# Kernel tuning notes

Hardware: AMD Instinct MI355X
Metric: run time of the kernel (lower is better)

## Reference

```python
import jax, jax.numpy as jnp
import numpy as np

B, C, G = 2, 256, 32
SPATIAL = (16, 16, 16)
EPS = 1e-5


def setup_inputs() -> dict:
    key = jax.random.key(0)
    ks = jax.random.split(key, 11)
    s = 1.0 / np.sqrt(C)
    x = jax.random.normal(ks[0], (B, C) + SPATIAL, dtype=jnp.float32)
    mk = lambda k: jax.random.normal(k, (C, C), dtype=jnp.float32) * s
    return {
        "x": x,
        "Wq": mk(ks[1]), "bq": jnp.zeros((C,), jnp.float32),
        "Wk": mk(ks[2]), "bk": jnp.zeros((C,), jnp.float32),
        "Wv": mk(ks[3]), "bv": jnp.zeros((C,), jnp.float32),
        "Wo": mk(ks[4]), "bo": jnp.zeros((C,), jnp.float32),
        "gamma": jnp.ones((C,), jnp.float32),
        "beta": jnp.zeros((C,), jnp.float32),
    }


def reference(x, Wq, bq, Wk, bk, Wv, bv, Wo, bo, gamma, beta):
    b, c = x.shape[0], x.shape[1]
    xf = x.reshape(b, c, -1)  # [B, C, N]

    def proj1x1(inp, W, bias):
        return jnp.einsum('oc,bcn->bon', W, inp) + bias[None, :, None]

    q = proj1x1(xf, Wq, bq)
    k = proj1x1(xf, Wk, bk)
    v = proj1x1(xf, Wv, bv)

    # qk[b, n, m] = sum_c q[b, c, n] * k[b, c, m]   (no 1/sqrt(C) scale, as in source)
    scores = jnp.einsum('bcn,bcm->bnm', q, k)
    w = jax.nn.softmax(scores, axis=-1)
    # h[b, c, n] = sum_m v[b, c, m] * w[b, n, m]
    h = jnp.einsum('bcm,bnm->bcn', v, w)
    h = proj1x1(h, Wo, bo)

    y = xf + h  # residual

    # GroupNorm over (channels-in-group, spatial)
    yg = y.reshape(b, G, c // G, -1)
    mu = jnp.mean(yg, axis=(2, 3), keepdims=True)
    var = jnp.var(yg, axis=(2, 3), keepdims=True)
    yn = ((yg - mu) * jax.lax.rsqrt(var + EPS)).reshape(b, c, -1)
    yn = yn * gamma[None, :, None] + beta[None, :, None]

    out = yn * jax.nn.sigmoid(yn)  # SiLU
    return out.reshape(x.shape)
```

## Files before the change

kernel.cpp:

```cpp
#include <hip/hip_runtime.h>
#include <hip/hip_bf16.h>

typedef _Float16 f16;
typedef __attribute__((ext_vector_type(4))) _Float16 f16x4;
typedef __attribute__((ext_vector_type(8))) _Float16 f16x8;
typedef __attribute__((ext_vector_type(4))) float f32x4;

#define CD 256
#define ND 4096
#define GD 32
#define KVB 32

__device__ __forceinline__ void gl_lds16(const f16* g, f16* l) {
    __builtin_amdgcn_global_load_lds(
        (const __attribute__((address_space(1))) unsigned int*)g,
        (__attribute__((address_space(3))) unsigned int*)l,
        16, 0, 0);
}

__global__ __launch_bounds__(256)
void k_proj_qkv(const float* __restrict__ x,
                const float* __restrict__ Wq, const float* __restrict__ bq,
                const float* __restrict__ Wk, const float* __restrict__ bk,
                const float* __restrict__ Wv, const float* __restrict__ bv,
                f16* __restrict__ Qt, f16* __restrict__ Kt, f16* __restrict__ Vb)
{
    __shared__ f16 As[3][64][40];
    __shared__ f16 Bs[64][40];
    __shared__ f16 Ts[64][72];

    const int t  = threadIdx.x;
    const int n0 = blockIdx.x * 64;
    const int o0 = blockIdx.y * 64;
    const int bb = blockIdx.z;

    const float* Ws[3] = { Wq, Wk, Wv };
    const float* bs[3] = { bq, bk, bv };

    const int w  = t >> 6;
    const int l  = t & 63;
    const int lr = l & 15;
    const int lg = l >> 4;
    const int wo = (w >> 1) * 32;
    const int wn = (w & 1) * 32;

    const int sl = t & 63;
    const int k8 = (t >> 6) * 8;

    f32x4 acc[3][2][2] = {};

    for (int ck = 0; ck < CD; ck += 32) {
        __syncthreads();
#pragma unroll
        for (int p = 0; p < 3; ++p) {
            const float* s = Ws[p] + (size_t)(o0 + sl) * CD + ck + k8;
            f16x8 v;
#pragma unroll
            for (int u = 0; u < 8; ++u) v[u] = (f16)s[u];
            *(f16x8*)&As[p][sl][k8] = v;
        }
        {
            const float* s = x + ((size_t)bb * CD + ck + k8) * ND + n0 + sl;
            f16x8 v;
#pragma unroll
            for (int u = 0; u < 8; ++u) v[u] = (f16)s[(size_t)u * ND];
            *(f16x8*)&Bs[sl][k8] = v;
        }
        __syncthreads();
        f16x8 b0 = *(const f16x8*)&Bs[wn + lr][lg * 8];
        f16x8 b1 = *(const f16x8*)&Bs[wn + 16 + lr][lg * 8];
#pragma unroll
        for (int p = 0; p < 3; ++p) {
            f16x8 a0 = *(const f16x8*)&As[p][wo + lr][lg * 8];
            f16x8 a1 = *(const f16x8*)&As[p][wo + 16 + lr][lg * 8];
            acc[p][0][0] = __builtin_amdgcn_mfma_f32_16x16x32_f16(a0, b0, acc[p][0][0], 0, 0, 0);
            acc[p][0][1] = __builtin_amdgcn_mfma_f32_16x16x32_f16(a0, b1, acc[p][0][1], 0, 0, 0);
            acc[p][1][0] = __builtin_amdgcn_mfma_f32_16x16x32_f16(a1, b0, acc[p][1][0], 0, 0, 0);
            acc[p][1][1] = __builtin_amdgcn_mfma_f32_16x16x32_f16(a1, b1, acc[p][1][1], 0, 0, 0);
        }
    }

#pragma unroll
    for (int p = 0; p < 2; ++p) {
        __syncthreads();
#pragma unroll
        for (int so = 0; so < 2; ++so)
#pragma unroll
            for (int r = 0; r < 4; ++r) {
                int orow  = wo + so * 16 + lg * 4 + r;
                float bv_ = bs[p][o0 + orow];
#pragma unroll
                for (int sn = 0; sn < 2; ++sn)
                    Ts[orow][wn + sn * 16 + lr] = (f16)(acc[p][so][sn][r] + bv_);
            }
        __syncthreads();
        f16* dst = (p == 0) ? Qt : Kt;
        int n  = t >> 2;
        int o8 = (t & 3) * 16;
        f16 tmp[16];
#pragma unroll
        for (int u = 0; u < 16; ++u) tmp[u] = Ts[o8 + u][n];
        f16* g = dst + ((size_t)bb * ND + n0 + n) * CD + o0 + o8;
        *(f16x8*)g       = *(f16x8*)&tmp[0];
        *(f16x8*)(g + 8) = *(f16x8*)&tmp[8];
    }
#pragma unroll
    for (int so = 0; so < 2; ++so)
#pragma unroll
        for (int r = 0; r < 4; ++r) {
            int orow  = wo + so * 16 + lg * 4 + r;
            float bv_ = bv[o0 + orow];
#pragma unroll
            for (int sn = 0; sn < 2; ++sn) {
                int ncol = wn + sn * 16 + lr;
                Vb[((size_t)bb * CD + o0 + orow) * ND + n0 + ncol] =
                    (f16)(acc[2][so][sn][r] + bv_);
            }
        }
}

template<int KSN>
__global__ __launch_bounds__(256, 2)
void k_attn(const f16* __restrict__ Qt, const f16* __restrict__ Kt,
            const f16* __restrict__ Vb, f16* __restrict__ Op,
            float* __restrict__ ml)
{
    __shared__ f16 Ks[2][32 * 256];
    __shared__ f16 Vs[2][256 * 32];
    __shared__ f16 Pl[4][32][40];

    const int t  = threadIdx.x;
    const int w  = t >> 6;
    const int l  = t & 63;
    const int lr = l & 15;
    const int lg = l >> 4;

    const int bid = blockIdx.x;
    int bb, ks, qi;
    if constexpr (KSN == 8) {
        int xcd = bid & 7;
        bb = xcd & 1;
        ks = (xcd >> 1) | ((bid >> 8) << 2);
        qi = (bid >> 3) & 31;
    } else {
        bb = bid & 1;
        ks = (bid >> 1) & 3;
        qi = bid >> 3;
    }
    const int q0 = qi * 128 + w * 32;

    f16x8 qf[2][8];
#pragma unroll
    for (int qs = 0; qs < 2; ++qs)
#pragma unroll
        for (int kc = 0; kc < 8; ++kc)
            qf[qs][kc] = *(const f16x8*)(Qt + ((size_t)bb * ND + q0 + qs * 16 + lr) * CD + kc * 32 + lg * 8);

    f32x4 oacc[2][16] = {};
    float row_m[2] = { -3.0e38f, -3.0e38f };
    float row_l[2] = { 0.f, 0.f };

    const int kv0 = ks * (ND / KSN);
    const f16* ktb = Kt + (size_t)bb * ND * CD;
    const f16* vbb = Vb + (size_t)bb * CD * ND;

    int koff[4], voff[4];
#pragma unroll
    for (int j = 0; j < 4; ++j) {
        int v   = (w * 4 + j) * 64 + l;
        int row = v >> 5;
        int ch  = (v & 31) ^ (row & 7);
        koff[j] = row * CD + ch * 8;
        int c   = v >> 2;
        int u   = (v & 3) ^ ((c >> 1) & 3);
        voff[j] = c * ND + u * 8;
    }

    auto stage = [&](int m0, int bi) {
#pragma unroll
        for (int j = 0; j < 4; ++j)
            gl_lds16(ktb + (size_t)m0 * CD + koff[j], &Ks[bi][(w * 4 + j) * 512]);
#pragma unroll
        for (int j = 0; j < 4; ++j)
            gl_lds16(vbb + m0 + voff[j], &Vs[bi][(w * 4 + j) * 512]);
    };

    stage(kv0, 0);
    __syncthreads();

    const int NIT = (ND / KSN) / KVB;
    for (int it = 0; it < NIT; ++it) {
        const int bi = it & 1;
        if (it + 1 < NIT) stage(kv0 + (it + 1) * KVB, bi ^ 1);

        f32x4 s[2][2] = {};
        __builtin_amdgcn_s_setprio(1);
#pragma unroll
        for (int kc = 0; kc < 8; ++kc) {
            int chs = ((kc * 4 + lg) ^ (lr & 7)) * 8;
            f16x8 k0 = *(const f16x8*)&Ks[bi][(lr) * 256 + chs];
            f16x8 k1 = *(const f16x8*)&Ks[bi][(16 + lr) * 256 + chs];
            s[0][0] = __builtin_amdgcn_mfma_f32_16x16x32_f16(k0, qf[0][kc], s[0][0], 0, 0, 0);
            s[1][0] = __builtin_amdgcn_mfma_f32_16x16x32_f16(k1, qf[0][kc], s[1][0], 0, 0, 0);
            s[0][1] = __builtin_amdgcn_mfma_f32_16x16x32_f16(k0, qf[1][kc], s[0][1], 0, 0, 0);
            s[1][1] = __builtin_amdgcn_mfma_f32_16x16x32_f16(k1, qf[1][kc], s[1][1], 0, 0, 0);
        }
        __builtin_amdgcn_s_setprio(0);

#pragma unroll
        for (int qs = 0; qs < 2; ++qs) {
            float pm = fmaxf(
                fmaxf(fmaxf(s[0][qs][0], s[0][qs][1]), fmaxf(s[0][qs][2], s[0][qs][3])),
                fmaxf(fmaxf(s[1][qs][0], s[1][qs][1]), fmaxf(s[1][qs][2], s[1][qs][3])));
            pm = fmaxf(pm, __shfl_xor(pm, 16));
            pm = fmaxf(pm, __shfl_xor(pm, 32));
            bool need = (pm > row_m[qs] + 5.0f);
            float nm  = need ? pm : row_m[qs];
            float p0 = __expf(s[0][qs][0] - nm);
            float p1 = __expf(s[0][qs][1] - nm);
            float p2 = __expf(s[0][qs][2] - nm);
            float p3 = __expf(s[0][qs][3] - nm);
            float p4 = __expf(s[1][qs][0] - nm);
            float p5 = __expf(s[1][qs][1] - nm);
            float p6 = __expf(s[1][qs][2] - nm);
            float p7 = __expf(s[1][qs][3] - nm);
            float ps = ((p0 + p1) + (p2 + p3)) + ((p4 + p5) + (p6 + p7));
            ps += __shfl_xor(ps, 16);
            ps += __shfl_xor(ps, 32);
            if (__any(need)) {
                float sc = __expf(row_m[qs] - nm);
                row_l[qs] = row_l[qs] * sc + ps;
#pragma unroll
                for (int ct = 0; ct < 16; ++ct) {
                    oacc[qs][ct][0] *= sc; oacc[qs][ct][1] *= sc;
                    oacc[qs][ct][2] *= sc; oacc[qs][ct][3] *= sc;
                }
            } else {
                row_l[qs] += ps;
            }
            row_m[qs] = nm;
            f16x4 pk0 = { (f16)p0, (f16)p1, (f16)p2, (f16)p3 };
            f16x4 pk1 = { (f16)p4, (f16)p5, (f16)p6, (f16)p7 };
            *(f16x4*)&Pl[w][qs * 16 + lr][lg * 4]      = pk0;
            *(f16x4*)&Pl[w][qs * 16 + lr][16 + lg * 4] = pk1;
        }

        f16x8 pf0 = *(const f16x8*)&Pl[w][lr][lg * 8];
        f16x8 pf1 = *(const f16x8*)&Pl[w][16 + lr][lg * 8];
        __builtin_amdgcn_s_setprio(1);
#pragma unroll
        for (int ct = 0; ct < 16; ++ct) {
            f16x8 vf = *(const f16x8*)&Vs[bi][(ct * 16 + lr) * 32 + ((lg ^ ((lr >> 1) & 3))) * 8];
            oacc[0][ct] = __builtin_amdgcn_mfma_f32_16x16x32_f16(vf, pf0, oacc[0][ct], 0, 0, 0);
            oacc[1][ct] = __builtin_amdgcn_mfma_f32_16x16x32_f16(vf, pf1, oacc[1][ct], 0, 0, 0);
        }
        __builtin_amdgcn_s_setprio(0);
        __syncthreads();
    }

#pragma unroll
    for (int qs = 0; qs < 2; ++qs)
#pragma unroll
        for (int ct = 0; ct < 16; ++ct)
#pragma unroll
            for (int r = 0; r < 4; ++r) {
                int cch = ct * 16 + lg * 4 + r;
                Op[(((size_t)ks * 2 + bb) * CD + cch) * ND + q0 + qs * 16 + lr] =
                    (f16)oacc[qs][ct][r];
            }
    if (lg == 0) {
#pragma unroll
        for (int qs = 0; qs < 2; ++qs) {
            int n = q0 + qs * 16 + lr;
            ml[((ks * 2 + bb) * 2 + 0) * ND + n] = row_m[qs];
            ml[((ks * 2 + bb) * 2 + 1) * ND + n] = row_l[qs];
        }
    }
}

template<int KSN>
__global__ __launch_bounds__(256)
void k_ml(const float* __restrict__ ml, float* __restrict__ wq)
{
    int i = blockIdx.x * 256 + threadIdx.x;
    int b = i / ND, n = i % ND;
    float m[KSN], lv[KSN];
#pragma unroll
    for (int ks = 0; ks < KSN; ++ks) {
        m[ks]  = ml[((ks * 2 + b) * 2 + 0) * ND + n];
        lv[ks] = ml[((ks * 2 + b) * 2 + 1) * ND + n];
    }
    float M = m[0];
#pragma unroll
    for (int ks = 1; ks < KSN; ++ks) M = fmaxf(M, m[ks]);
    float wgt[KSN], L = 0.f;
#pragma unroll
    for (int ks = 0; ks < KSN; ++ks) { wgt[ks] = __expf(m[ks] - M); L += wgt[ks] * lv[ks]; }
    float inv = 1.0f / L;
#pragma unroll
    for (int ks = 0; ks < KSN; ++ks)
        wq[(ks * 2 + b) * ND + n] = wgt[ks] * inv;
}

template<int KSN>
__global__ __launch_bounds__(256)
void k_comb(const f16* __restrict__ Op, const float* __restrict__ wq,
            f16* __restrict__ Hb)
{
    size_t i = (size_t)blockIdx.x * 256 + threadIdx.x;
    int n0 = (int)(i % (ND / 8)) * 8;
    int c  = (int)((i / (ND / 8)) % CD);
    int b  = (int)(i / ((size_t)CD * (ND / 8)));

    float acc[8] = {};
#pragma unroll
    for (int ks = 0; ks < KSN; ++ks) {
        f16x8 o = *(const f16x8*)(Op + (((size_t)ks * 2 + b) * CD + c) * ND + n0);
        const float* wp = wq + (ks * 2 + b) * ND + n0;
        float4 w0 = *(const float4*)wp;
        float4 w1 = *(const float4*)(wp + 4);
        acc[0] += w0.x * (float)o[0]; acc[1] += w0.y * (float)o[1];
        acc[2] += w0.z * (float)o[2]; acc[3] += w0.w * (float)o[3];
        acc[4] += w1.x * (float)o[4]; acc[5] += w1.y * (float)o[5];
        acc[6] += w1.z * (float)o[6]; acc[7] += w1.w * (float)o[7];
    }
    f16x8 h;
#pragma unroll
    for (int u = 0; u < 8; ++u) h[u] = (f16)acc[u];
    *(f16x8*)(Hb + ((size_t)b * CD + c) * ND + n0) = h;
}

__global__ __launch_bounds__(256)
void k_proj_o(const f16* __restrict__ Hb, const float* __restrict__ Wo,
              const float* __restrict__ bo, const float* __restrict__ x,
              f16* __restrict__ Yh, float* __restrict__ part)
{
    __shared__ f16 As[64][40];
    __shared__ f16 Bs[64][40];
    __shared__ float rs[4][2][2][2];

    const int t  = threadIdx.x;
    const int n0 = blockIdx.x * 64;
    const int o0 = blockIdx.y * 64;
    const int bb = blockIdx.z;

    const int w  = t >> 6;
    const int l  = t & 63;
    const int lr = l & 15;
    const int lg = l >> 4;
    const int wo = (w >> 1) * 32;
    const int wn = (w & 1) * 32;

    const int sl = t & 63;
    const int k8 = (t >> 6) * 8;

    f32x4 acc[2][2] = {};

    for (int ck = 0; ck < CD; ck += 32) {
        __syncthreads();
        {
            const float* s = Wo + (size_t)(o0 + sl) * CD + ck + k8;
            f16x8 v;
#pragma unroll
            for (int u = 0; u < 8; ++u) v[u] = (f16)s[u];
            *(f16x8*)&As[sl][k8] = v;
        }
        {
            const f16* s = Hb + ((size_t)bb * CD + ck + k8) * ND + n0 + sl;
            f16x8 v;
#pragma unroll
            for (int u = 0; u < 8; ++u) v[u] = s[(size_t)u * ND];
            *(f16x8*)&Bs[sl][k8] = v;
        }
        __syncthreads();
        f16x8 a0 = *(const f16x8*)&As[wo + lr][lg * 8];
        f16x8 a1 = *(const f16x8*)&As[wo + 16 + lr][lg * 8];
        f16x8 b0 = *(const f16x8*)&Bs[wn + lr][lg * 8];
        f16x8 b1 = *(const f16x8*)&Bs[wn + 16 + lr][lg * 8];
        acc[0][0] = __builtin_amdgcn_mfma_f32_16x16x32_f16(a0, b0, acc[0][0], 0, 0, 0);
        acc[0][1] = __builtin_amdgcn_mfma_f32_16x16x32_f16(a0, b1, acc[0][1], 0, 0, 0);
        acc[1][0] = __builtin_amdgcn_mfma_f32_16x16x32_f16(a1, b0, acc[1][0], 0, 0, 0);
        acc[1][1] = __builtin_amdgcn_mfma_f32_16x16x32_f16(a1, b1, acc[1][1], 0, 0, 0);
    }

#pragma unroll
    for (int so = 0; so < 2; ++so) {
        float ls = 0.f, ls2 = 0.f;
#pragma unroll
        for (int r = 0; r < 4; ++r) {
            int orow  = wo + so * 16 + lg * 4 + r;
            float bv_ = bo[o0 + orow];
#pragma unroll
            for (int sn = 0; sn < 2; ++sn) {
                int ncol   = wn + sn * 16 + lr;
                size_t idx = ((size_t)bb * CD + o0 + orow) * ND + n0 + ncol;
                float v = acc[so][sn][r] + bv_ + x[idx];
                Yh[idx] = (f16)v;
                ls  += v;
                ls2 += v * v;
            }
        }
#pragma unroll
        for (int m = 1; m <= 16; m <<= 1) {
            ls  += __shfl_xor(ls, m);
            ls2 += __shfl_xor(ls2, m);
        }
        if ((l & 31) == 0) {
            rs[w][so][l >> 5][0] = ls;
            rs[w][so][l >> 5][1] = ls2;
        }
    }
    __syncthreads();
    if (t < 16) {
        int gl = t >> 1, st = t & 1;
        int a = gl >> 2, so = (gl >> 1) & 1, lh = gl & 1;
        float v = rs[2 * a][so][lh][st] + rs[2 * a + 1][so][lh][st];
        part[(((size_t)bb * GD + (o0 >> 3) + gl) * 64 + blockIdx.x) * 2 + st] = v;
    }
}

__global__ __launch_bounds__(256)
void k_gn_silu(const f16* __restrict__ Yh, const float* __restrict__ part,
               const float* __restrict__ gamma, const float* __restrict__ beta,
               float* __restrict__ out)
{
    const int g  = blockIdx.x, b = blockIdx.y, nq = blockIdx.z;
    const int t  = threadIdx.x;

    __shared__ float mr[2];
    if (t < 64) {
        float s  = part[(((size_t)b * GD + g) * 64 + t) * 2 + 0];
        float s2 = part[(((size_t)b * GD + g) * 64 + t) * 2 + 1];
#pragma unroll
        for (int m = 1; m < 64; m <<= 1) {
            s  += __shfl_xor(s, m);
            s2 += __shfl_xor(s2, m);
        }
        if (t == 0) {
            float mean = s / 32768.f;
            float var  = s2 / 32768.f - mean * mean;
            mr[0] = mean;
            mr[1] = rsqrtf(var + 1e-5f);
        }
    }
    __syncthreads();
    const float mean = mr[0], rstd = mr[1];

    const size_t base = ((size_t)b * CD + g * 8) * ND;
    const f16x8* src = (const f16x8*)(Yh + base);

    for (int i = t; i < 1024; i += 256) {
        int ch = i >> 7;
        int nn = i & 127;
        f16x8 v = src[ch * (ND / 8) + nq * 128 + nn];
        int c = g * 8 + ch;
        float ga = gamma[c], be = beta[c];
        float ob[8];
#pragma unroll
        for (int u = 0; u < 8; ++u) {
            float yn = ((float)v[u] - mean) * rstd * ga + be;
            float sg = 1.0f / (1.0f + __expf(-yn));
            ob[u] = yn * sg;
        }
        float* dp = out + base + (size_t)ch * ND + nq * 1024 + nn * 8;
        *(float4*)dp       = *(float4*)&ob[0];
        *(float4*)(dp + 4) = *(float4*)&ob[4];
    }
}

extern "C" void kernel_launch(void* const* d_in, const int* in_sizes, int n_in,
                              void* d_out, int out_size, void* d_ws, size_t ws_size,
                              hipStream_t stream)
{
    const float* x     = (const float*)d_in[0];
    const float* Wq    = (const float*)d_in[1];
    const float* bq    = (const float*)d_in[2];
    const float* Wk    = (const float*)d_in[3];
    const float* bk    = (const float*)d_in[4];
    const float* Wv    = (const float*)d_in[5];
    const float* bv    = (const float*)d_in[6];
    const float* Wo    = (const float*)d_in[7];
    const float* bo    = (const float*)d_in[8];
    const float* gamma = (const float*)d_in[9];
    const float* beta  = (const float*)d_in[10];

    char* ws = (char*)d_ws;
    f16* Qt = (f16*)(ws);
    f16* Kt = (f16*)(ws + (4u << 20));
    f16* Vb = (f16*)(ws + (8u << 20));
    f16* Hb = (f16*)(ws + (12u << 20));
    f16* Op = (f16*)(ws + (16u << 20));
    f16* Yh = (f16*)(ws + (16u << 20));

    const bool big = ws_size >= (50ull << 20);

    k_proj_qkv<<<dim3(64, 4, 2), 256, 0, stream>>>(x, Wq, bq, Wk, bk, Wv, bv, Qt, Kt, Vb);

    if (big) {
        constexpr int KSN = 8;
        float* ml   = (float*)(ws + (48u << 20));
        float* wq   = (float*)(ws + (48u << 20) + (768u << 10));
        float* part = (float*)(ws + (49u << 20) + (512u << 10));
        k_attn<KSN><<<dim3(32 * KSN * 2), 256, 0, stream>>>(Qt, Kt, Vb, Op, ml);
        k_ml<KSN><<<dim3((2 * ND) / 256), 256, 0, stream>>>(ml, wq);
        k_comb<KSN><<<dim3((2 * CD * ND / 8) / 256), 256, 0, stream>>>(Op, wq, Hb);
        k_proj_o<<<dim3(64, 4, 2), 256, 0, stream>>>(Hb, Wo, bo, x, Yh, part);
        k_gn_silu<<<dim3(GD, 2, 4), 256, 0, stream>>>(Yh, part, gamma, beta, (float*)d_out);
    } else {
        constexpr int KSN = 4;
        float* ml   = (float*)(ws + (32u << 20));
        float* wq   = (float*)(ws + (32u << 20) + (512u << 10));
        float* part = (float*)(ws + (33u << 20));
        k_attn<KSN><<<dim3(32 * KSN * 2), 256, 0, stream>>>(Qt, Kt, Vb, Op, ml);
        k_ml<KSN><<<dim3((2 * ND) / 256), 256, 0, stream>>>(ml, wq);
        k_comb<KSN><<<dim3((2 * CD * ND / 8) / 256), 256, 0, stream>>>(Op, wq, Hb);
        k_proj_o<<<dim3(64, 4, 2), 256, 0, stream>>>(Hb, Wo, bo, x, Yh, part);
        k_gn_silu<<<dim3(GD, 2, 4), 256, 0, stream>>>(Yh, part, gamma, beta, (float*)d_out);
    }
}
```

Before: 104.9 us.

## Switch attention kernel to 32x32x16 MFMA and pass P through registers

The flash-attention kernel now uses 32x32x16 MFMA tiles instead of 16x16x32, so each wave handles its 32 queries as one tile. Softmax needs only a single cross-half shuffle per row, and the probability matrix is packed with cvt_pkrtz and exchanged via lane shuffles rather than a round trip through LDS. This removes the Pl shared buffer and its LDS writes and reads, and lowers shuffle overhead. In exchange, accumulators become 16-wide vectors, which raises register pressure, and the P values are rounded toward zero.

Result: slower. 111.9 us (+6.7%).

```diff
diff --git a/kernel.cpp b/kernel.cpp
--- a/kernel.cpp
+++ b/kernel.cpp
@@ -2,9 +2,12 @@
 #include <hip/hip_bf16.h>
 
 typedef _Float16 f16;
+typedef __attribute__((ext_vector_type(2))) __fp16 h16x2;
 typedef __attribute__((ext_vector_type(4))) _Float16 f16x4;
 typedef __attribute__((ext_vector_type(8))) _Float16 f16x8;
 typedef __attribute__((ext_vector_type(4))) float f32x4;
+typedef __attribute__((ext_vector_type(16))) float f32x16;
+typedef __attribute__((ext_vector_type(4))) unsigned int u32x4;
 
 #define CD 256
 #define ND 4096
@@ -127,13 +130,12 @@
 {
     __shared__ f16 Ks[2][32 * 256];
     __shared__ f16 Vs[2][256 * 32];
-    __shared__ f16 Pl[4][32][40];
-
-    const int t  = threadIdx.x;
-    const int w  = t >> 6;
-    const int l  = t & 63;
-    const int lr = l & 15;
-    const int lg = l >> 4;
+
+    const int t   = threadIdx.x;
+    const int w   = t >> 6;
+    const int l   = t & 63;
+    const int q32 = l & 31;
+    const int hi  = l >> 5;
 
     const int bid = blockIdx.x;
     int bb, ks, qi;
@@ -149,16 +151,13 @@
     }
     const int q0 = qi * 128 + w * 32;
 
-    f16x8 qf[2][8];
-#pragma unroll
-    for (int qs = 0; qs < 2; ++qs)
-#pragma unroll
-        for (int kc = 0; kc < 8; ++kc)
-            qf[qs][kc] = *(const f16x8*)(Qt + ((size_t)bb * ND + q0 + qs * 16 + lr) * CD + kc * 32 + lg * 8);
-
-    f32x4 oacc[2][16] = {};
-    float row_m[2] = { -3.0e38f, -3.0e38f };
-    float row_l[2] = { 0.f, 0.f };
+    f16x8 qf[16];
+#pragma unroll
+    for (int n = 0; n < 16; ++n)
+        qf[n] = *(const f16x8*)(Qt + ((size_t)bb * ND + q0 + q32) * CD + n * 16 + hi * 8);
+
+    f32x16 oacc[8] = {};
+    float row_m = -3.0e38f, row_l = 0.f;
 
     const int kv0 = ks * (ND / KSN);
     const f16* ktb = Kt + (size_t)bb * ND * CD;
@@ -193,88 +192,92 @@
         const int bi = it & 1;
         if (it + 1 < NIT) stage(kv0 + (it + 1) * KVB, bi ^ 1);
 
-        f32x4 s[2][2] = {};
+        f32x16 sa = {}, sb = {};
         __builtin_amdgcn_s_setprio(1);
 #pragma unroll
-        for (int kc = 0; kc < 8; ++kc) {
-            int chs = ((kc * 4 + lg) ^ (lr & 7)) * 8;
-            f16x8 k0 = *(const f16x8*)&Ks[bi][(lr) * 256 + chs];
-            f16x8 k1 = *(const f16x8*)&Ks[bi][(16 + lr) * 256 + chs];
-            s[0][0] = __builtin_amdgcn_mfma_f32_16x16x32_f16(k0, qf[0][kc], s[0][0], 0, 0, 0);
-            s[1][0] = __builtin_amdgcn_mfma_f32_16x16x32_f16(k1, qf[0][kc], s[1][0], 0, 0, 0);
-            s[0][1] = __builtin_amdgcn_mfma_f32_16x16x32_f16(k0, qf[1][kc], s[0][1], 0, 0, 0);
-            s[1][1] = __builtin_amdgcn_mfma_f32_16x16x32_f16(k1, qf[1][kc], s[1][1], 0, 0, 0);
+        for (int n = 0; n < 16; n += 2) {
+            f16x8 ka = *(const f16x8*)&Ks[bi][q32 * 256 + (((2 * n + hi) ^ (q32 & 7))) * 8];
+            f16x8 kb = *(const f16x8*)&Ks[bi][q32 * 256 + (((2 * n + 2 + hi) ^ (q32 & 7))) * 8];
+            sa = __builtin_amdgcn_mfma_f32_32x32x16_f16(ka, qf[n],     sa, 0, 0, 0);
+            sb = __builtin_amdgcn_mfma_f32_32x32x16_f16(kb, qf[n + 1], sb, 0, 0, 0);
         }
         __builtin_amdgcn_s_setprio(0);
 
-#pragma unroll
-        for (int qs = 0; qs < 2; ++qs) {
-            float pm = fmaxf(
-                fmaxf(fmaxf(s[0][qs][0], s[0][qs][1]), fmaxf(s[0][qs][2], s[0][qs][3])),
-                fmaxf(fmaxf(s[1][qs][0], s[1][qs][1]), fmaxf(s[1][qs][2], s[1][qs][3])));
-            pm = fmaxf(pm, __shfl_xor(pm, 16));
-            pm = fmaxf(pm, __shfl_xor(pm, 32));
-            bool need = (pm > row_m[qs] + 5.0f);
-            float nm  = need ? pm : row_m[qs];
-            float p0 = __expf(s[0][qs][0] - nm);
-            float p1 = __expf(s[0][qs][1] - nm);
-            float p2 = __expf(s[0][qs][2] - nm);
-            float p3 = __expf(s[0][qs][3] - nm);
-            float p4 = __expf(s[1][qs][0] - nm);
-            float p5 = __expf(s[1][qs][1] - nm);
-            float p6 = __expf(s[1][qs][2] - nm);
-            float p7 = __expf(s[1][qs][3] - nm);
-            float ps = ((p0 + p1) + (p2 + p3)) + ((p4 + p5) + (p6 + p7));
-            ps += __shfl_xor(ps, 16);
-            ps += __shfl_xor(ps, 32);
-            if (__any(need)) {
-                float sc = __expf(row_m[qs] - nm);
-                row_l[qs] = row_l[qs] * sc + ps;
-#pragma unroll
-                for (int ct = 0; ct < 16; ++ct) {
-                    oacc[qs][ct][0] *= sc; oacc[qs][ct][1] *= sc;
-                    oacc[qs][ct][2] *= sc; oacc[qs][ct][3] *= sc;
-                }
-            } else {
-                row_l[qs] += ps;
-            }
-            row_m[qs] = nm;
-            f16x4 pk0 = { (f16)p0, (f16)p1, (f16)p2, (f16)p3 };
-            f16x4 pk1 = { (f16)p4, (f16)p5, (f16)p6, (f16)p7 };
-            *(f16x4*)&Pl[w][qs * 16 + lr][lg * 4]      = pk0;
-            *(f16x4*)&Pl[w][qs * 16 + lr][16 + lg * 4] = pk1;
-        }
-
-        f16x8 pf0 = *(const f16x8*)&Pl[w][lr][lg * 8];
-        f16x8 pf1 = *(const f16x8*)&Pl[w][16 + lr][lg * 8];
+        float s[16];
+#pragma unroll
+        for (int r = 0; r < 16; ++r) s[r] = sa[r] + sb[r];
+
+        float pm = s[0];
+#pragma unroll
+        for (int r = 1; r < 16; ++r) pm = fmaxf(pm, s[r]);
+        pm = fmaxf(pm, __shfl_xor(pm, 32));
+        bool need = (pm > row_m + 5.0f);
+        float nm  = need ? pm : row_m;
+        float p[16];
+#pragma unroll
+        for (int r = 0; r < 16; ++r) p[r] = __expf(s[r] - nm);
+        float ps = 0.f;
+#pragma unroll
+        for (int r = 0; r < 16; ++r) ps += p[r];
+        ps += __shfl_xor(ps, 32);
+        if (__any(need)) {
+            float sc = __expf(row_m - nm);
+            row_l = row_l * sc + ps;
+#pragma unroll
+            for (int cc = 0; cc < 8; ++cc)
+#pragma unroll
+                for (int r = 0; r < 16; ++r) oacc[cc][r] *= sc;
+        } else {
+            row_l += ps;
+        }
+        row_m = nm;
+
+        unsigned int wv[8], ov[8];
+#pragma unroll
+        for (int c = 0; c < 4; ++c) {
+            h16x2 a = __builtin_amdgcn_cvt_pkrtz(p[4 * c],     p[4 * c + 1]);
+            h16x2 b = __builtin_amdgcn_cvt_pkrtz(p[4 * c + 2], p[4 * c + 3]);
+            wv[2 * c]     = __builtin_bit_cast(unsigned int, a);
+            wv[2 * c + 1] = __builtin_bit_cast(unsigned int, b);
+        }
+#pragma unroll
+        for (int i = 0; i < 8; ++i) ov[i] = __shfl_xor(wv[i], 32);
+        f16x8 pb[2];
+#pragma unroll
+        for (int j = 0; j < 2; ++j) {
+            u32x4 bwords;
+            bwords[0] = hi ? ov[4 * j + 2] : wv[4 * j];
+            bwords[1] = hi ? ov[4 * j + 3] : wv[4 * j + 1];
+            bwords[2] = hi ? wv[4 * j + 2] : ov[4 * j];
+            bwords[3] = hi ? wv[4 * j + 3] : ov[4 * j + 1];
+            pb[j] = __builtin_bit_cast(f16x8, bwords);
+        }
+
         __builtin_amdgcn_s_setprio(1);
 #pragma unroll
-        for (int ct = 0; ct < 16; ++ct) {
-            f16x8 vf = *(const f16x8*)&Vs[bi][(ct * 16 + lr) * 32 + ((lg ^ ((lr >> 1) & 3))) * 8];
-            oacc[0][ct] = __builtin_amdgcn_mfma_f32_16x16x32_f16(vf, pf0, oacc[0][ct], 0, 0, 0);
-            oacc[1][ct] = __builtin_amdgcn_mfma_f32_16x16x32_f16(vf, pf1, oacc[1][ct], 0, 0, 0);
+        for (int cc = 0; cc < 8; ++cc) {
+            int crow = cc * 32 + q32;
+            int sw   = (crow >> 1) & 3;
+            f16x8 v0 = *(const f16x8*)&Vs[bi][crow * 32 + ((hi       ^ sw)) * 8];
+            f16x8 v1 = *(const f16x8*)&Vs[bi][crow * 32 + (((2 + hi) ^ sw)) * 8];
+            oacc[cc] = __builtin_amdgcn_mfma_f32_32x32x16_f16(v0, pb[0], oacc[cc], 0, 0, 0);
+            oacc[cc] = __builtin_amdgcn_mfma_f32_32x32x16_f16(v1, pb[1], oacc[cc], 0, 0, 0);
         }
         __builtin_amdgcn_s_setprio(0);
         __syncthreads();
     }
 
 #pragma unroll
-    for (int qs = 0; qs < 2; ++qs)
-#pragma unroll
-        for (int ct = 0; ct < 16; ++ct)
-#pragma unroll
-            for (int r = 0; r < 4; ++r) {
-                int cch = ct * 16 + lg * 4 + r;
-                Op[(((size_t)ks * 2 + bb) * CD + cch) * ND + q0 + qs * 16 + lr] =
-                    (f16)oacc[qs][ct][r];
-            }
-    if (lg == 0) {
-#pragma unroll
-        for (int qs = 0; qs < 2; ++qs) {
-            int n = q0 + qs * 16 + lr;
-            ml[((ks * 2 + bb) * 2 + 0) * ND + n] = row_m[qs];
-            ml[((ks * 2 + bb) * 2 + 1) * ND + n] = row_l[qs];
-        }
+    for (int cc = 0; cc < 8; ++cc)
+#pragma unroll
+        for (int r = 0; r < 16; ++r) {
+            int cch = cc * 32 + (r & 3) + 8 * (r >> 2) + 4 * hi;
+            Op[(((size_t)ks * 2 + bb) * CD + cch) * ND + q0 + q32] = (f16)oacc[cc][r];
+        }
+    if (l < 32) {
+        int n = q0 + l;
+        ml[((ks * 2 + bb) * 2 + 0) * ND + n] = row_m;
+        ml[((ks * 2 + bb) * 2 + 1) * ND + n] = row_l;
     }
 }
 
```
